# Kernel optimization log

Measured on AMD Instinct MI355X. Metric: run time of the kernel, lower is better.

## Reference

```python
import jax, jax.numpy as jnp
import numpy as np

N_NODES = 50000
N_EDGES = 800000
D_FEAT = 128
EMBED = 128
HEADS = 8
HEAD_DIM = EMBED // HEADS


def setup_inputs() -> dict:
    key = jax.random.key(0)
    ks = jax.random.split(key, 10)
    xavier = jax.nn.initializers.xavier_normal()
    return {
        "nodes": jax.random.normal(ks[0], (N_NODES, D_FEAT), jnp.float32),
        "edges": jax.random.normal(ks[1], (N_EDGES, D_FEAT), jnp.float32),
        "senders": jax.random.randint(ks[2], (N_EDGES,), 0, N_NODES, jnp.int32),
        "receivers": jax.random.randint(ks[3], (N_EDGES,), 0, N_NODES, jnp.int32),
        "Ws_k": xavier(ks[4], (D_FEAT, EMBED), jnp.float32),
        "Ws_b": jnp.zeros((EMBED,), jnp.float32),
        "Wr_k": xavier(ks[5], (D_FEAT, EMBED), jnp.float32),
        "Wr_b": jnp.zeros((EMBED,), jnp.float32),
        "We_k": xavier(ks[6], (D_FEAT, EMBED), jnp.float32),
        "We_b": jnp.zeros((EMBED,), jnp.float32),
        "a": xavier(ks[7], (HEADS, HEAD_DIM), jnp.float32),
    }


def reference(nodes, edges, senders, receivers, Ws_k, Ws_b, Wr_k, Wr_b, We_k, We_b, a):
    N = nodes.shape[0]
    E = edges.shape[0]
    H, D = a.shape
    # Node-level projections (linear, so equivalent to projecting gathered edge endpoints)
    hs = nodes @ Ws_k + Ws_b            # [N, HD]  (W_s on sent attributes)
    hr = nodes @ Wr_k + Wr_b            # [N, HD]  (W_r on received attributes)
    he = edges @ We_k + We_b            # [E, HD]  (W_e on edge attributes)
    sent = hs[senders]                  # [E, HD]
    x = jax.nn.leaky_relu(sent + hr[receivers] + he)  # default slope 0.01, as original
    xh = x.reshape(E, H, D)
    logits = jnp.sum(xh * a, axis=-1)   # [E, H]
    # segment_softmax over receivers (stable: subtract per-segment max)
    mx = jax.ops.segment_max(logits, receivers, num_segments=N)  # [N, H]
    mx = jnp.where(jnp.isfinite(mx), mx, 0.0)
    ex = jnp.exp(logits - mx[receivers])                         # [E, H]
    denom = jax.ops.segment_sum(ex, receivers, num_segments=N)   # [N, H]
    w = ex / denom[receivers]                                    # [E, H]
    msg = (w[..., None] * sent.reshape(E, H, D)).reshape(E, H * D)
    out = jax.ops.segment_sum(msg, receivers, num_segments=N)    # [N, HD]
    return out
```

## Files before the change

kernel.cpp:

```cpp
#include <hip/hip_runtime.h>

#define N_NODES 50000
#define N_EDGES 800000
#define D 128
#define HEADS 8

typedef __attribute__((ext_vector_type(8))) short short8b;
typedef __attribute__((ext_vector_type(4))) float f32x4;

__device__ __forceinline__ unsigned short f2bf_rne(float f) {
    unsigned int u = __float_as_uint(f);
    u += 0x7FFFu + ((u >> 16) & 1u);
    return (unsigned short)(u >> 16);
}
__device__ __forceinline__ float bf2f(unsigned short u) {
    return __uint_as_float(((unsigned int)u) << 16);
}

template <int CTRL>
__device__ __forceinline__ float dpp_radd(float v) {
    int s = __builtin_amdgcn_update_dpp(0, __float_as_int(v), CTRL, 0xF, 0xF, true);
    return v + __int_as_float(s);
}
__device__ __forceinline__ float rowsum16(float v) {
    v = dpp_radd<0xB1>(v);
    v = dpp_radd<0x4E>(v);
    v = dpp_radd<0x141>(v);
    v = dpp_radd<0x140>(v);
    return v;
}

#define K1_ROWS 128
#define K1_TILES ((N_NODES + K1_ROWS - 1) / K1_ROWS)

__device__ __forceinline__ void proj_body(
    int tile, const float* __restrict__ nodes,
    const float* __restrict__ W, const float* __restrict__ bias,
    unsigned short* __restrict__ outp)
{
    __shared__ __align__(16) unsigned short WT[D][136];
    __shared__ __align__(16) unsigned short At[64][136];
    int t = threadIdx.x;
    int lane = t & 63;
    int wv = t >> 6;
    int lg = lane >> 4;
    int li = lane & 15;

    #pragma unroll 8
    for (int j = 0; j < 64; ++j) {
        int idx = t + 256 * j;
        int k = idx >> 7, c = idx & 127;
        WT[c][k] = f2bf_rne(W[idx]);
    }
    float b_ct[8];
    #pragma unroll
    for (int ct = 0; ct < 8; ++ct) b_ct[ct] = bias[ct * 16 + li];

    #pragma unroll 1
    for (int sub = 0; sub < 2; ++sub) {
        int row0 = tile * K1_ROWS + sub * 64;
        if (row0 >= N_NODES) break;
        __syncthreads();
        {
            const float4* Nv = (const float4*)nodes;
            #pragma unroll
            for (int j = 0; j < 8; ++j) {
                int fi = t + 256 * j;
                int r = row0 + (fi >> 5);
                float4 v = make_float4(0.f, 0.f, 0.f, 0.f);
                if (r < N_NODES) v = Nv[(size_t)r * 32 + (fi & 31)];
                ushort4 b;
                b.x = f2bf_rne(v.x); b.y = f2bf_rne(v.y);
                b.z = f2bf_rne(v.z); b.w = f2bf_rne(v.w);
                *(ushort4*)&At[fi >> 5][(fi & 31) * 4] = b;
            }
        }
        __syncthreads();

        short8b afr[4];
        #pragma unroll
        for (int kb = 0; kb < 4; ++kb)
            afr[kb] = *(const short8b*)&At[wv * 16 + li][kb * 32 + lg * 8];

        #pragma unroll
        for (int ct = 0; ct < 8; ++ct) {
            f32x4 acc = {0.f, 0.f, 0.f, 0.f};
            #pragma unroll
            for (int kb = 0; kb < 4; ++kb) {
                short8b bfr = *(const short8b*)&WT[ct * 16 + li][kb * 32 + lg * 8];
                acc = __builtin_amdgcn_mfma_f32_16x16x32_bf16(afr[kb], bfr, acc, 0, 0, 0);
            }
            #pragma unroll
            for (int j = 0; j < 4; ++j) {
                int r = row0 + wv * 16 + lg * 4 + j;
                if (r < N_NODES)
                    outp[(size_t)r * D + ct * 16 + li] = f2bf_rne(acc[j] + b_ct[ct]);
            }
        }
    }
}

__global__ __launch_bounds__(256, 3) void k_projS_hist(
    const float* __restrict__ nodes,
    const float* __restrict__ Ws, const float* __restrict__ bs,
    unsigned short* __restrict__ hsb,
    const int* __restrict__ receivers, int* __restrict__ deg)
{
    int bx = blockIdx.x;
    if (bx < K1_TILES) {
        proj_body(bx, nodes, Ws, bs, hsb);
    } else {
        int i = (bx - K1_TILES) * 256 + threadIdx.x;
        if (i < N_EDGES) atomicAdd(&deg[receivers[i]], 1);
    }
}

#define SCAN_CHUNK 49
__global__ __launch_bounds__(1024) void k_scan(
    const int* __restrict__ deg, int* __restrict__ rowptr, int* __restrict__ cursor)
{
    __shared__ int sm[1024];
    int t = threadIdx.x;
    int base = t * SCAN_CHUNK;
    int lsum = 0;
    #pragma unroll 4
    for (int i = 0; i < SCAN_CHUNK; ++i) {
        int idx = base + i;
        if (idx < N_NODES) lsum += deg[idx];
    }
    sm[t] = lsum;
    __syncthreads();
    for (int off = 1; off < 1024; off <<= 1) {
        int v = (t >= off) ? sm[t - off] : 0;
        __syncthreads();
        sm[t] += v;
        __syncthreads();
    }
    int run = (t > 0) ? sm[t - 1] : 0;
    for (int i = 0; i < SCAN_CHUNK; ++i) {
        int idx = base + i;
        if (idx < N_NODES) {
            rowptr[idx] = run;
            cursor[idx] = run;
            run += deg[idx];
        }
    }
    if (t == 1023) rowptr[N_NODES] = sm[1023];
}

__global__ __launch_bounds__(256, 3) void k_projR_fill(
    const float* __restrict__ nodes,
    const float* __restrict__ Wr, const float* __restrict__ br,
    unsigned short* __restrict__ hrb,
    const int* __restrict__ receivers, const int* __restrict__ senders,
    int* __restrict__ cursor,
    int* __restrict__ s_csr, int* __restrict__ pos_csr)
{
    int bx = blockIdx.x;
    if (bx < K1_TILES) {
        proj_body(bx, nodes, Wr, br, hrb);
    } else {
        int i = (bx - K1_TILES) * 256 + threadIdx.x;
        if (i < N_EDGES) {
            int r = receivers[i];
            int pos = atomicAdd(&cursor[r], 1);
            s_csr[pos]  = senders[i];
            pos_csr[i]  = pos;
        }
    }
}

#define BLK_E 64
__global__ __launch_bounds__(256, 3) void k_edge_logits_mfma(
    const float* __restrict__ edges,
    const int* __restrict__ senders, const int* __restrict__ receivers,
    const int* __restrict__ pos_csr,
    const float* __restrict__ We, const float* __restrict__ be,
    const float* __restrict__ a,
    const unsigned short* __restrict__ hsb, const unsigned short* __restrict__ hrb,
    float* __restrict__ ex)
{
    __shared__ __align__(16) unsigned short WeT[D][136];
    __shared__ __align__(16) unsigned short Et[BLK_E][136];
    int t = threadIdx.x;
    int lane = t & 63;
    int wv = t >> 6;
    int lg = lane >> 4;
    int li = lane & 15;

    #pragma unroll 8
    for (int j = 0; j < 64; ++j) {
        int idx = t + 256 * j;
        int k = idx >> 7, c = idx & 127;
        WeT[c][k] = f2bf_rne(We[idx]);
    }
    float a_h[HEADS], be_h[HEADS];
    #pragma unroll
    for (int h = 0; h < HEADS; ++h) {
        a_h[h]  = a[h * 16 + li];
        be_h[h] = be[h * 16 + li];
    }
    __syncthreads();

    const int ntiles = N_EDGES / BLK_E;
    const float4* Ev = (const float4*)edges;

    for (int tile = blockIdx.x; tile < ntiles; tile += gridDim.x) {
        int pb = tile * BLK_E + wv * 16;

        #pragma unroll
        for (int j = 0; j < 8; ++j) {
            int fi = lane + 64 * j;
            int rloc = fi >> 5;
            float4 v = Ev[(size_t)(pb + rloc) * 32 + (fi & 31)];
            ushort4 b;
            b.x = f2bf_rne(v.x); b.y = f2bf_rne(v.y);
            b.z = f2bf_rne(v.z); b.w = f2bf_rne(v.w);
            *(ushort4*)&Et[wv * 16 + rloc][(fi & 31) * 4] = b;
        }

        int sj[4], rj[4];
        #pragma unroll
        for (int j = 0; j < 4; ++j) {
            sj[j] = senders[pb + lg * 4 + j];
            rj[j] = receivers[pb + lg * 4 + j];
        }
        int o = 4 * lg + (li >> 2);
        int mypos = pos_csr[pb + o];

        unsigned short g_hs[4][HEADS], g_hr[4][HEADS];
        #pragma unroll
        for (int j = 0; j < 4; ++j) {
            const unsigned short* hsrow = hsb + (size_t)sj[j] * D + li;
            const unsigned short* hrrow = hrb + (size_t)rj[j] * D + li;
            #pragma unroll
            for (int h = 0; h < HEADS; ++h) {
                g_hs[j][h] = hsrow[h * 16];
                g_hr[j][h] = hrrow[h * 16];
            }
        }

        asm volatile("s_waitcnt lgkmcnt(0)" ::: "memory");
        __builtin_amdgcn_sched_barrier(0);

        short8b afr[4];
        #pragma unroll
        for (int kb = 0; kb < 4; ++kb)
            afr[kb] = *(const short8b*)&Et[wv * 16 + li][kb * 32 + lg * 8];

        float hold[8];
        #pragma unroll
        for (int h = 0; h < HEADS; ++h) {
            f32x4 acc = {0.f, 0.f, 0.f, 0.f};
            #pragma unroll
            for (int kb = 0; kb < 4; ++kb) {
                short8b bfr = *(const short8b*)&WeT[h * 16 + li][kb * 32 + lg * 8];
                acc = __builtin_amdgcn_mfma_f32_16x16x32_bf16(afr[kb], bfr, acc, 0, 0, 0);
            }
            float pr[4];
            #pragma unroll
            for (int j = 0; j < 4; ++j) {
                float x = acc[j] + be_h[h] + bf2f(g_hs[j][h]) + bf2f(g_hr[j][h]);
                x = fmaxf(x, 0.01f * x);
                pr[j] = rowsum16(x * a_h[h]);
            }
            float qa = (li & 4) ? pr[1] : pr[0];
            float qb = (li & 4) ? pr[3] : pr[2];
            hold[h] = __expf((li & 8) ? qb : qa);
        }
        {
            float a0 = (li & 1) ? hold[2] : hold[0];
            float a1 = (li & 1) ? hold[6] : hold[4];
            float ea = (li & 2) ? a1 : a0;
            float b0 = (li & 1) ? hold[3] : hold[1];
            float b1 = (li & 1) ? hold[7] : hold[5];
            float eb = (li & 2) ? b1 : b0;
            int h1 = 2 * (li & 3);
            *(float2*)&ex[(size_t)mypos * HEADS + h1] = make_float2(ea, eb);
        }
        __builtin_amdgcn_wave_barrier();
    }
}

__global__ __launch_bounds__(256) void k_gather_out(
    const int* __restrict__ rowptr, const int* __restrict__ s_csr,
    const unsigned short* __restrict__ hsb, const float* __restrict__ ex,
    float* __restrict__ out)
{
    int r = blockIdx.x * 4 + (threadIdx.x >> 6);
    int l = threadIdx.x & 63;
    int h = l >> 3;
    int beg = rowptr[r], end = rowptr[r + 1];

    float2 acc = make_float2(0.f, 0.f);
    float dsum = 0.f;
    for (int j0 = beg; j0 < end; j0 += 16) {
        int cnt = end - j0;
        int s[16]; float w[16];
        #pragma unroll
        for (int q = 0; q < 16; ++q)
            if (q < cnt) { s[q] = s_csr[j0 + q]; w[q] = ex[(size_t)(j0 + q) * HEADS + h]; }
        #pragma unroll
        for (int q = 0; q < 16; ++q)
            if (q < cnt) {
                ushort2 hv = *(const ushort2*)&hsb[(size_t)s[q] * D + 2 * l];
                acc.x += w[q] * bf2f(hv.x);
                acc.y += w[q] * bf2f(hv.y);
                dsum  += w[q];
            }
    }
    float inv = (end > beg && dsum != 0.f) ? (1.0f / dsum) : 0.f;
    acc.x *= inv; acc.y *= inv;
    *(float2*)&out[(size_t)r * D + 2 * l] = acc;
}

extern "C" void kernel_launch(void* const* d_in, const int* in_sizes, int n_in,
                              void* d_out, int out_size, void* d_ws, size_t ws_size,
                              hipStream_t stream) {
    const float* nodes     = (const float*)d_in[0];
    const float* edges     = (const float*)d_in[1];
    const int*   senders   = (const int*)d_in[2];
    const int*   receivers = (const int*)d_in[3];
    const float* Ws = (const float*)d_in[4];
    const float* bs = (const float*)d_in[5];
    const float* Wr = (const float*)d_in[6];
    const float* br = (const float*)d_in[7];
    const float* We = (const float*)d_in[8];
    const float* be = (const float*)d_in[9];
    const float* a  = (const float*)d_in[10];
    float* out = (float*)d_out;

    unsigned short* hsb = (unsigned short*)d_ws;
    unsigned short* hrb = hsb + (size_t)N_NODES * D;
    float* ex    = (float*)(hrb + (size_t)N_NODES * D);
    int* deg     = (int*)(ex + (size_t)N_EDGES * HEADS);
    int* rowptr  = deg + N_NODES;
    int* cursor  = rowptr + N_NODES + 1;
    int* s_csr   = cursor + N_NODES;
    int* pos_csr = s_csr + N_EDGES;

    const int HIST_BLKS = N_EDGES / 256;

    (void)hipMemsetAsync(deg, 0, N_NODES * sizeof(int), stream);
    k_projS_hist<<<K1_TILES + HIST_BLKS, 256, 0, stream>>>(
        nodes, Ws, bs, hsb, receivers, deg);
    k_scan<<<1, 1024, 0, stream>>>(deg, rowptr, cursor);
    k_projR_fill<<<K1_TILES + HIST_BLKS, 256, 0, stream>>>(
        nodes, Wr, br, hrb, receivers, senders, cursor, s_csr, pos_csr);
    k_edge_logits_mfma<<<2500, 256, 0, stream>>>(edges, senders, receivers, pos_csr,
                                                 We, be, a, hsb, hrb, ex);
    k_gather_out<<<N_NODES / 4, 256, 0, stream>>>(rowptr, s_csr, hsb, ex, out);
}
```

Baseline: 405.4 us.

## Permute bf16 projection layout so per-lane head values gather as 16-byte vectors

The node projection kernel now writes each row of hs/hr in a head-interleaved order (column li*8+head) using one 16-byte packed store per row, instead of eight scattered 2-byte stores. This lets the edge kernel fetch all eight head values for its lane with a single vector load per endpoint, instead of eight scalar 2-byte gathers. The output-aggregation kernel is adapted to the permuted layout: it reads paired attention weights as float2, keeps two softmax denominators, and un-permutes the result through a small shared-memory buffer before the coalesced store. This trades some extra LDS traffic and register pressure for far fewer scattered global loads.

```diff
diff --git a/kernel.cpp b/kernel.cpp
--- a/kernel.cpp
+++ b/kernel.cpp
@@ -6,6 +6,7 @@
 #define HEADS 8
 
 typedef __attribute__((ext_vector_type(8))) short short8b;
+typedef __attribute__((ext_vector_type(8))) unsigned short ushort8v;
 typedef __attribute__((ext_vector_type(4))) float f32x4;
 
 __device__ __forceinline__ unsigned short f2bf_rne(float f) {
@@ -82,6 +83,7 @@
         for (int kb = 0; kb < 4; ++kb)
             afr[kb] = *(const short8b*)&At[wv * 16 + li][kb * 32 + lg * 8];
 
+        f32x4 accs[8];
         #pragma unroll
         for (int ct = 0; ct < 8; ++ct) {
             f32x4 acc = {0.f, 0.f, 0.f, 0.f};
@@ -90,11 +92,22 @@
                 short8b bfr = *(const short8b*)&WT[ct * 16 + li][kb * 32 + lg * 8];
                 acc = __builtin_amdgcn_mfma_f32_16x16x32_bf16(afr[kb], bfr, acc, 0, 0, 0);
             }
-            #pragma unroll
-            for (int j = 0; j < 4; ++j) {
-                int r = row0 + wv * 16 + lg * 4 + j;
-                if (r < N_NODES)
-                    outp[(size_t)r * D + ct * 16 + li] = f2bf_rne(acc[j] + b_ct[ct]);
+            accs[ct] = acc;
+        }
+        #pragma unroll
+        for (int j = 0; j < 4; ++j) {
+            int r = row0 + wv * 16 + lg * 4 + j;
+            if (r < N_NODES) {
+                uint4 w;
+                w.x = (unsigned)f2bf_rne(accs[0][j] + b_ct[0])
+                    | ((unsigned)f2bf_rne(accs[1][j] + b_ct[1]) << 16);
+                w.y = (unsigned)f2bf_rne(accs[2][j] + b_ct[2])
+                    | ((unsigned)f2bf_rne(accs[3][j] + b_ct[3]) << 16);
+                w.z = (unsigned)f2bf_rne(accs[4][j] + b_ct[4])
+                    | ((unsigned)f2bf_rne(accs[5][j] + b_ct[5]) << 16);
+                w.w = (unsigned)f2bf_rne(accs[6][j] + b_ct[6])
+                    | ((unsigned)f2bf_rne(accs[7][j] + b_ct[7]) << 16);
+                *(uint4*)&outp[(size_t)r * D + li * 8] = w;
             }
         }
     }
@@ -228,16 +241,11 @@
         int o = 4 * lg + (li >> 2);
         int mypos = pos_csr[pb + o];
 
-        unsigned short g_hs[4][HEADS], g_hr[4][HEADS];
+        ushort8v g_hs[4], g_hr[4];
         #pragma unroll
         for (int j = 0; j < 4; ++j) {
-            const unsigned short* hsrow = hsb + (size_t)sj[j] * D + li;
-            const unsigned short* hrrow = hrb + (size_t)rj[j] * D + li;
-            #pragma unroll
-            for (int h = 0; h < HEADS; ++h) {
-                g_hs[j][h] = hsrow[h * 16];
-                g_hr[j][h] = hrrow[h * 16];
-            }
+            g_hs[j] = *(const ushort8v*)(hsb + (size_t)sj[j] * D + li * 8);
+            g_hr[j] = *(const ushort8v*)(hrb + (size_t)rj[j] * D + li * 8);
         }
 
         asm volatile("s_waitcnt lgkmcnt(0)" ::: "memory");
@@ -287,31 +295,43 @@
     const unsigned short* __restrict__ hsb, const float* __restrict__ ex,
     float* __restrict__ out)
 {
-    int r = blockIdx.x * 4 + (threadIdx.x >> 6);
+    __shared__ float obuf[4][128];
+    int wvid = threadIdx.x >> 6;
+    int r = blockIdx.x * 4 + wvid;
     int l = threadIdx.x & 63;
-    int h = l >> 3;
+    int h1 = 2 * (l & 3);
+    int c1 = (l >> 2) + 16 * h1;
     int beg = rowptr[r], end = rowptr[r + 1];
 
     float2 acc = make_float2(0.f, 0.f);
-    float dsum = 0.f;
+    float ds1 = 0.f, ds2 = 0.f;
     for (int j0 = beg; j0 < end; j0 += 16) {
         int cnt = end - j0;
-        int s[16]; float w[16];
+        int s[16]; float2 w2[16];
         #pragma unroll
         for (int q = 0; q < 16; ++q)
-            if (q < cnt) { s[q] = s_csr[j0 + q]; w[q] = ex[(size_t)(j0 + q) * HEADS + h]; }
+            if (q < cnt) {
+                s[q]  = s_csr[j0 + q];
+                w2[q] = *(const float2*)&ex[(size_t)(j0 + q) * HEADS + h1];
+            }
         #pragma unroll
         for (int q = 0; q < 16; ++q)
             if (q < cnt) {
                 ushort2 hv = *(const ushort2*)&hsb[(size_t)s[q] * D + 2 * l];
-                acc.x += w[q] * bf2f(hv.x);
-                acc.y += w[q] * bf2f(hv.y);
-                dsum  += w[q];
-            }
-    }
-    float inv = (end > beg && dsum != 0.f) ? (1.0f / dsum) : 0.f;
-    acc.x *= inv; acc.y *= inv;
-    *(float2*)&out[(size_t)r * D + 2 * l] = acc;
+                acc.x += w2[q].x * bf2f(hv.x);
+                acc.y += w2[q].y * bf2f(hv.y);
+                ds1   += w2[q].x;
+                ds2   += w2[q].y;
+            }
+    }
+    float i1 = (end > beg && ds1 != 0.f) ? (1.0f / ds1) : 0.f;
+    float i2 = (end > beg && ds2 != 0.f) ? (1.0f / ds2) : 0.f;
+    obuf[wvid][c1]      = acc.x * i1;
+    obuf[wvid][c1 + 16] = acc.y * i2;
+    asm volatile("s_waitcnt lgkmcnt(0)" ::: "memory");
+    __builtin_amdgcn_sched_barrier(0);
+    float2 o2 = *(const float2*)&obuf[wvid][2 * l];
+    *(float2*)&out[(size_t)r * D + 2 * l] = o2;
 }
 
 extern "C" void kernel_launch(void* const* d_in, const int* in_sizes, int n_in,
```

Result: slower. 451.9 us (+11.5%).
